# Kernel optimization log

Measured on AMD Instinct MI355X. Metric: run time of the kernel, lower is better.

Reference implementation:

```python
import jax, jax.numpy as jnp
import numpy as np

EXP_SCALE = 10.0   # self.exp_param_scale
BETA_UP = 5.0      # self.kernel_beta_upbound
N_HEAD = 12


def setup_inputs() -> dict:
    key = jax.random.key(0)
    ks = jax.random.split(key, 7)
    B, T, C, nh = 2, 2048, 768, N_HEAD
    s = 1.0 / np.sqrt(C)
    x = jax.random.normal(ks[0], (B, T, C), jnp.float32)
    W_la = jax.random.normal(ks[1], (C, C), jnp.float32) * s      # LeakyAverage linear
    la_coef = jax.random.uniform(ks[2], (nh,), jnp.float32)        # per-head leaky decay in (0,1)
    W_v = jax.random.normal(ks[3], (C, C), jnp.float32) * s        # v_featurizer linear
    v_coef = jax.random.uniform(ks[4], (nh,), jnp.float32)         # v_featurizer per-head coef
    kernel_beta = jnp.ones((nh,), jnp.float32) / EXP_SCALE
    value_beta = jnp.ones((nh,), jnp.float32) * (-0.5 / EXP_SCALE)
    W_proj = jax.random.normal(ks[5], (C, C), jnp.float32) * s     # c_proj
    return dict(x=x, W_la=W_la, la_coef=la_coef, W_v=W_v, v_coef=v_coef,
                kernel_beta=kernel_beta, value_beta=value_beta, W_proj=W_proj)


def _leaky_average(x, W_la, la_coef):
    # y_t = c * y_{t-1} + (1-c) * (x W^T)_t, per-head decay c. Returns (B, nh, T, hs).
    B, T, C = x.shape
    nh = la_coef.shape[0]
    hs = C // nh
    u = (x @ W_la.T).reshape(B, T, nh, hs)
    c = la_coef[None, :, None]  # (1, nh, 1) broadcast over (B, nh, hs)

    def step(carry, ut):
        y = c * carry + (1.0 - c) * ut
        return y, y

    _, ys = jax.lax.scan(step, jnp.zeros((B, nh, hs), x.dtype), jnp.swapaxes(u, 0, 1))
    return jnp.transpose(ys, (1, 2, 0, 3))  # (T,B,nh,hs) -> (B,nh,T,hs)


def reference(x, W_la, la_coef, W_v, v_coef, kernel_beta, value_beta, W_proj):
    B, T, C = x.shape
    nh = la_coef.shape[0]
    hs = C // nh
    v_shift = 1

    # K path: leaky-average features, L2-normalize, exp-kernel beta scale
    k0 = _leaky_average(x, W_la, la_coef)                               # (B,nh,T,hs)
    raw_k = k0 / (jnp.linalg.norm(k0, axis=-1, keepdims=True) + 1e-6)
    beta = jnp.exp(jnp.minimum(kernel_beta * EXP_SCALE, BETA_UP))
    k = raw_k * beta[None, :, None, None]

    # V path: lowrlinearconv featurizer (linear, shift-by-1 mix, normalize) + value scale
    xl = (x @ W_v.T).reshape(B, T, nh, hs).transpose(0, 2, 1, 3)        # (B,nh,T,hs)
    shifted = jnp.concatenate([xl[:, :, 1:], jnp.zeros_like(xl[:, :, :1])], axis=2)
    vc = v_coef[None, :, None, None]
    vf = shifted * (1.0 - vc) + xl * vc
    vf = vf / (jnp.linalg.norm(vf, axis=-1, keepdims=True) + 1e-6)
    vbeta = jnp.exp(jnp.minimum(value_beta * EXP_SCALE, BETA_UP))
    v = vf * vbeta[None, :, None, None]

    # shifted-causal attention: query at position t (t>=1) attends keys 0..t-1, scale=1.0
    q = k[:, :, v_shift:]                                               # (B,nh,T-1,hs)
    scores = jnp.einsum('bhqd,bhkd->bhqk', q, k)                        # (B,nh,T-1,T)
    mask = jnp.tril(jnp.ones((T - v_shift, T), bool))                   # j <= iq  <=>  key < query pos
    scores = jnp.where(mask, scores, -jnp.inf)
    attn = jax.nn.softmax(scores, axis=-1)
    o = jnp.einsum('bhqk,bhkd->bhqd', attn, v)
    y = jnp.concatenate([jnp.zeros((B, nh, v_shift, hs), x.dtype), o], axis=2)

    y = y.transpose(0, 2, 1, 3).reshape(B, T, C)
    return y @ W_proj.T  # c_proj (dropouts are identity in eval)
```

## Files before the change

kernel.cpp:

```cpp
#include <hip/hip_runtime.h>
#include <hip/hip_bf16.h>
#include <math.h>

#define B_   2
#define T_   2048
#define C_   768
#define NH   12
#define HS   64
#define NSEG 64
#define SEGLEN 32
#define CX   1536

typedef __attribute__((ext_vector_type(8))) short short8;
typedef __attribute__((ext_vector_type(4))) short short4v;
typedef __attribute__((ext_vector_type(4))) float f32x4;

static __device__ inline unsigned short f2b(float f) {
  __hip_bfloat16 h = __float2bfloat16(f);
  unsigned short u;
  __builtin_memcpy(&u, &h, 2);
  return u;
}

#define GLOAD_LDS16(gp, lp)                                                        \
  __builtin_amdgcn_global_load_lds((const __attribute__((address_space(1))) void*)(gp), \
                                   (__attribute__((address_space(3))) void*)(lp), 16, 0, 0)

__global__ __launch_bounds__(256) void cast_all(const float* __restrict__ x,
                                                const float* __restrict__ wla,
                                                const float* __restrict__ wv,
                                                const float* __restrict__ wp,
                                                __hip_bfloat16* __restrict__ xb,
                                                __hip_bfloat16* __restrict__ wcat,
                                                __hip_bfloat16* __restrict__ wpb) {
  const int NX4 = (B_ * T_ * C_) / 4;
  const int NW4 = (C_ * C_) / 4;
  const int TOT = NX4 + 3 * NW4;
  int i = blockIdx.x * 256 + threadIdx.x;
  int st = gridDim.x * 256;
  for (; i < TOT; i += st) {
    const float* s;
    unsigned short* d;
    if (i < NX4) { s = x + (size_t)i * 4; d = (unsigned short*)xb + (size_t)i * 4; }
    else if (i < NX4 + NW4) { int j = i - NX4; s = wla + (size_t)j * 4; d = (unsigned short*)wcat + (size_t)j * 4; }
    else if (i < NX4 + 2 * NW4) { int j = i - NX4 - NW4; s = wv + (size_t)j * 4; d = (unsigned short*)wcat + (size_t)(C_ * C_) + (size_t)j * 4; }
    else { int j = i - NX4 - 2 * NW4; s = wp + (size_t)j * 4; d = (unsigned short*)wpb + (size_t)j * 4; }
    float4 v = *(const float4*)s;
    short4v o;
    o.x = (short)f2b(v.x); o.y = (short)f2b(v.y); o.z = (short)f2b(v.z); o.w = (short)f2b(v.w);
    *(short4v*)d = o;
  }
}

template <int BM>
__global__ __launch_bounds__(256) void gemm_bf16(const __hip_bfloat16* __restrict__ A,
                                                 const __hip_bfloat16* __restrict__ Bw,
                                                 float* __restrict__ C,
                                                 int M, int N, int K) {
  __shared__ __hip_bfloat16 As[BM * 64];
  __shared__ __hip_bfloat16 Bs[128 * 64];
  const int tid = threadIdx.x;
  const int w = tid >> 6, lane = tid & 63;
  const int bm = blockIdx.x * BM, bn = blockIdx.y * 128;
  const int q16 = lane & 15, lg = lane >> 4;

  constexpr int NACC = (BM == 128) ? 4 : 2;
  f32x4 acc[4][NACC];
#pragma unroll
  for (int i = 0; i < 4; ++i)
#pragma unroll
    for (int j = 0; j < NACC; ++j) acc[i][j] = (f32x4){0.f, 0.f, 0.f, 0.f};

  const int srow = (lane >> 3);
  const int soff0 = (lane & 7) * 16;
  const int sw = (lane & 7) << 4;
  constexpr int ACH = BM / 8;
  constexpr int CPW = (ACH + 16) / 4;

  for (int k0 = 0; k0 < K; k0 += 64) {
    __syncthreads();
#pragma unroll
    for (int c = 0; c < CPW; ++c) {
      int gc = w * CPW + c;
      int isB = gc >= ACH;
      int ci = isB ? gc - ACH : gc;
      int row = ci * 8 + srow;
      int soff = soff0 ^ ((row & 7) << 4);
      const __hip_bfloat16* gp =
          (isB ? Bw + (size_t)(bn + row) * K : A + (size_t)(bm + row) * K) + k0 + (soff >> 1);
      __hip_bfloat16* lp = (isB ? Bs : As) + ci * 512;
      GLOAD_LDS16(gp, lp);
    }
    __syncthreads();
#pragma unroll
    for (int ks = 0; ks < 2; ++ks) {
      short8 af[4], bf[NACC];
      const int colb = ks * 64 + lg * 16;
#pragma unroll
      for (int i = 0; i < 4; ++i) {
        int ra = (BM == 128) ? ((w >> 1) * 64 + i * 16 + q16) : (i * 16 + q16);
        af[i] = *(const short8*)((const char*)As + ra * 128 + (colb ^ sw));
      }
#pragma unroll
      for (int j = 0; j < NACC; ++j) {
        int rb = (BM == 128) ? ((w & 1) * 64 + j * 16 + q16) : (w * 32 + j * 16 + q16);
        bf[j] = *(const short8*)((const char*)Bs + rb * 128 + (colb ^ sw));
      }
#pragma unroll
      for (int i = 0; i < 4; ++i)
#pragma unroll
        for (int j = 0; j < NACC; ++j)
          acc[i][j] = __builtin_amdgcn_mfma_f32_16x16x32_bf16(af[i], bf[j], acc[i][j], 0, 0, 0);
    }
  }
#pragma unroll
  for (int i = 0; i < 4; ++i) {
#pragma unroll
    for (int r = 0; r < 4; ++r) {
      int m = (BM == 128) ? (bm + (w >> 1) * 64 + i * 16 + lg * 4 + r)
                          : (bm + i * 16 + lg * 4 + r);
      int nb = (BM == 128) ? (bn + (w & 1) * 64 + q16) : (bn + w * 32 + q16);
      float* cp = C + (size_t)m * N + nb;
#pragma unroll
      for (int j = 0; j < NACC; ++j) cp[j * 16] = acc[i][j][r];
    }
  }
}

__global__ __launch_bounds__(256) void scan_seg(const float* __restrict__ uxv,
                                                const float* __restrict__ la_coef,
                                                float* __restrict__ segend) {
  int cid = blockIdx.x * 4 + (threadIdx.x >> 6);
  int d   = threadIdx.x & 63;
  int seg = cid & (NSEG - 1);
  int bh  = cid >> 6;
  int h   = bh % NH;
  int b   = bh / NH;
  float c  = la_coef[h];
  float oc = 1.f - c;
  int t0 = seg * SEGLEN;
  const float* up = uxv + ((size_t)b * T_ + t0) * CX + h * HS + d;
  float y = 0.f;
  for (int i = 0; i < SEGLEN; ++i)
    y = fmaf(c, y, oc * up[(size_t)i * CX]);
  segend[(size_t)cid * HS + d] = y;
}

__global__ __launch_bounds__(256) void scan_b(const float* __restrict__ la_coef,
                                              const float* __restrict__ segend,
                                              float* __restrict__ carryin) {
  int s = blockIdx.x * 256 + threadIdx.x;
  if (s >= B_ * NH * HS) return;
  int d  = s & 63;
  int bh = s >> 6;
  int h  = bh % NH;
  float c = la_coef[h];
  float cl = c;
#pragma unroll
  for (int i = 0; i < 5; ++i) cl *= cl;
  float h0 = 0.f;
  for (int seg = 0; seg < NSEG; ++seg) {
    int cid = bh * NSEG + seg;
    carryin[(size_t)cid * HS + d] = h0;
    h0 = fmaf(cl, h0, segend[(size_t)cid * HS + d]);
  }
}

__global__ __launch_bounds__(256) void scan_c_norm(const float* __restrict__ la_coef,
                                                   const float* __restrict__ kernel_beta,
                                                   const float* __restrict__ carryin,
                                                   const float* __restrict__ uxv,
                                                   __hip_bfloat16* __restrict__ kb16) {
  int cid = blockIdx.x * 4 + (threadIdx.x >> 6);
  int d   = threadIdx.x & 63;
  int seg = cid & (NSEG - 1);
  int bh  = cid >> 6;
  int h   = bh % NH;
  int b   = bh / NH;
  float c  = la_coef[h];
  float oc = 1.f - c;
  float bk = __expf(fminf(kernel_beta[h] * 10.f, 5.f));
  int t0 = seg * SEGLEN;
  const float* up = uxv + ((size_t)b * T_ + t0) * CX + h * HS + d;
  __hip_bfloat16* op = kb16 + ((size_t)bh * T_ + t0) * HS + d;
  float y = carryin[(size_t)cid * HS + d];
  for (int i = 0; i < SEGLEN; ++i) {
    y = fmaf(c, y, oc * up[(size_t)i * CX]);
    float ss = y * y;
#pragma unroll
    for (int off = 1; off < 64; off <<= 1) ss += __shfl_xor(ss, off, 64);
    float scale = bk / (sqrtf(ss) + 1e-6f);
    op[(size_t)i * HS] = __float2bfloat16(y * scale);
  }
}

__global__ __launch_bounds__(256) void vbuild_t(const float* __restrict__ uxv,
                                                const float* __restrict__ v_coef,
                                                const float* __restrict__ value_beta,
                                                __hip_bfloat16* __restrict__ vt) {
  __shared__ __hip_bfloat16 sm[64][73];
  int t0 = blockIdx.x * 64;
  int bh = blockIdx.y;
  int h = bh % NH, b = bh / NH;
  int w = threadIdx.x >> 6, lane = threadIdx.x & 63;
  float vc = v_coef[h];
  float vb = __expf(fminf(value_beta[h] * 10.f, 5.f));
  for (int i = 0; i < 16; ++i) {
    int tl = w * 16 + i;
    int t = t0 + tl;
    const float* xp = uxv + ((size_t)b * T_ + t) * CX + 768 + h * HS + lane;
    float x0 = *xp;
    float x1 = (t + 1 < T_) ? xp[CX] : 0.f;
    float vf = (1.f - vc) * x1 + vc * x0;
    float ss = vf * vf;
#pragma unroll
    for (int off = 1; off < 64; off <<= 1) ss += __shfl_xor(ss, off, 64);
    sm[tl][lane] = __float2bfloat16(vf * vb / (sqrtf(ss) + 1e-6f));
  }
  __syncthreads();
  int d = threadIdx.x >> 3;
  int c = threadIdx.x & 7;
  for (int i = 0; i < 2; ++i) {
    int dd = d + i * 32;
    short8 v;
#pragma unroll
    for (int k = 0; k < 8; ++k)
      v[k] = (short)((const unsigned short*)&sm[c * 8 + k][dd])[0];
    *(short8*)((unsigned short*)vt + ((size_t)bh * HS + dd) * T_ + t0 + c * 8) = v;
  }
}

__global__ __launch_bounds__(256, 4) void attn7(const __hip_bfloat16* __restrict__ Kg,
                                                const __hip_bfloat16* __restrict__ Vtg,
                                                const float* __restrict__ kernel_beta,
                                                __hip_bfloat16* __restrict__ Y) {
  __shared__ __hip_bfloat16 Kt[2][64 * 64];
  __shared__ __hip_bfloat16 Vt[3][64 * 64];
  __shared__ char Pl[4][2304];
  const int bh = blockIdx.x;
  const int b = bh / NH, h = bh % NH;
  const int w = threadIdx.x >> 6, lane = threadIdx.x & 63;
  const int q16 = lane & 15, lg = lane >> 4;
  const int it = 31 - blockIdx.y;
  const int qb0 = 1 + it * 64;
  float bk = __expf(fminf(kernel_beta[h] * 10.f, 5.f));
  float m0 = bk * bk;
  const unsigned short* Kh = (const unsigned short*)Kg + (size_t)bh * T_ * HS;
  const unsigned short* Vh = (const unsigned short*)Vtg + (size_t)bh * HS * T_;
  unsigned short* Yh = (unsigned short*)Y + (size_t)b * T_ * C_ + h * HS;

  if (it == 0 && w == 0) Yh[lane] = 0;

  const int tq = qb0 + w * 16 + q16;
  short8 qf[2];
  {
    int tqc = tq > T_ - 1 ? T_ - 1 : tq;
#pragma unroll
    for (int ks = 0; ks < 2; ++ks)
      qf[ks] = *(const short8*)(Kh + (size_t)tqc * HS + ks * 32 + lg * 8);
  }

  f32x4 zero = {0.f, 0.f, 0.f, 0.f};
  f32x4 accO[4];
#pragma unroll
  for (int mt = 0; mt < 4; ++mt) accO[mt] = zero;
  float lsum = 0.f;
  f32x4 sp[4];

  char* pb = &Pl[w][0] + q16 * 144;
  const int swr = (q16 & 7) << 4;

  const int srow = lane >> 3;
  const int soff = ((lane & 7) << 4) ^ (srow << 4);

  const int NT = (qb0 + 126) >> 6;

#define STAGE_KV(kbuf, vbuf, j0)                                                      \
  {                                                                                   \
    _Pragma("unroll")                                                                 \
    for (int n = 0; n < 2; ++n) {                                                     \
      int ch = w * 2 + n;                                                             \
      int row = ch * 8 + srow;                                                        \
      GLOAD_LDS16((const char*)(Kh + (size_t)((j0) + row) * HS) + soff,               \
                  &Kt[kbuf][ch * 512]);                                               \
      GLOAD_LDS16((const char*)(Vh + (size_t)row * T_ + (j0)) + soff,                 \
                  &Vt[vbuf][ch * 512]);                                               \
    }                                                                                 \
  }

#define SM_PV(tp)                                                                     \
  {                                                                                   \
    const int j0p = (tp)*64;                                                          \
    const char* Vb = (const char*)&Vt[(tp) % 3][0];                                   \
    _Pragma("unroll")                                                                 \
    for (int nt = 0; nt < 4; ++nt) {                                                  \
      float p[4];                                                                     \
      _Pragma("unroll")                                                               \
      for (int r = 0; r < 4; ++r) {                                                   \
        int j = j0p + nt * 16 + lg * 4 + r;                                           \
        p[r] = (j < tq) ? __expf(sp[nt][r] - m0) : 0.f;                               \
        lsum += p[r];                                                                 \
      }                                                                               \
      unsigned int w0, w1;                                                            \
      asm("v_cvt_pk_bf16_f32 %0, %1, %2" : "=v"(w0) : "v"(p[0]), "v"(p[1]));          \
      asm("v_cvt_pk_bf16_f32 %0, %1, %2" : "=v"(w1) : "v"(p[2]), "v"(p[3]));          \
      uint2 pk; pk.x = w0; pk.y = w1;                                                 \
      *(uint2*)(pb + nt * 32 + lg * 8) = pk;                                          \
    }                                                                                 \
    __builtin_amdgcn_s_setprio(1);                                                    \
    _Pragma("unroll")                                                                 \
    for (int ks = 0; ks < 2; ++ks) {                                                  \
      short8 pf = *(const short8*)(pb + ks * 64 + lg * 16);                           \
      _Pragma("unroll")                                                               \
      for (int mt = 0; mt < 4; ++mt) {                                                \
        short8 vf = *(const short8*)(Vb + (mt * 16 + q16) * 128 +                     \
                                     ((ks * 64 + lg * 16) ^ swr));                    \
        accO[mt] = __builtin_amdgcn_mfma_f32_16x16x32_bf16(vf, pf, accO[mt], 0, 0, 0);\
      }                                                                               \
    }                                                                                 \
    __builtin_amdgcn_s_setprio(0);                                                    \
  }

  STAGE_KV(0, 0, 0);

  for (int kt = 0; kt < NT; ++kt) {
    const int j0 = kt * 64;
    if (kt + 1 < NT) {
      STAGE_KV((kt + 1) & 1, (kt + 1) % 3, j0 + 64);
      asm volatile("s_waitcnt vmcnt(4)" ::: "memory");
    } else {
      asm volatile("s_waitcnt vmcnt(0)" ::: "memory");
    }
    __builtin_amdgcn_s_barrier();
    __builtin_amdgcn_sched_barrier(0);

    const char* Kb = (const char*)&Kt[kt & 1][0];
    short8 kf[4][2];
#pragma unroll
    for (int nt = 0; nt < 4; ++nt)
#pragma unroll
      for (int ks = 0; ks < 2; ++ks)
        kf[nt][ks] = *(const short8*)(Kb + (nt * 16 + q16) * 128 + ((ks * 64 + lg * 16) ^ swr));
    f32x4 sc[4];
    __builtin_amdgcn_s_setprio(1);
#pragma unroll
    for (int nt = 0; nt < 4; ++nt) {
      sc[nt] = __builtin_amdgcn_mfma_f32_16x16x32_bf16(kf[nt][0], qf[0], zero, 0, 0, 0);
      sc[nt] = __builtin_amdgcn_mfma_f32_16x16x32_bf16(kf[nt][1], qf[1], sc[nt], 0, 0, 0);
    }
    __builtin_amdgcn_s_setprio(0);

    if (kt > 0) SM_PV(kt - 1);

#pragma unroll
    for (int nt = 0; nt < 4; ++nt) sp[nt] = sc[nt];

    asm volatile("s_waitcnt lgkmcnt(0)" ::: "memory");
    __builtin_amdgcn_s_barrier();
  }
  SM_PV(NT - 1);

  {
    float v = lsum;
    v += __shfl_xor(v, 16, 64);
    v += __shfl_xor(v, 32, 64);
    float inv = 1.f / v;
    if (tq < T_) {
      unsigned short* yp = Yh + (size_t)tq * C_;
#pragma unroll
      for (int mt = 0; mt < 4; ++mt) {
        float o0 = accO[mt][0] * inv, o1 = accO[mt][1] * inv;
        float o2 = accO[mt][2] * inv, o3 = accO[mt][3] * inv;
        unsigned int u0, u1;
        asm("v_cvt_pk_bf16_f32 %0, %1, %2" : "=v"(u0) : "v"(o0), "v"(o1));
        asm("v_cvt_pk_bf16_f32 %0, %1, %2" : "=v"(u1) : "v"(o2), "v"(o3));
        uint2 pk; pk.x = u0; pk.y = u1;
        *(uint2*)(yp + mt * 16 + lg * 4) = pk;
      }
    }
  }
#undef STAGE_KV
#undef SM_PV
}

extern "C" void kernel_launch(void* const* d_in, const int* in_sizes, int n_in,
                              void* d_out, int out_size, void* d_ws, size_t ws_size,
                              hipStream_t stream) {
  const float* x          = (const float*)d_in[0];
  const float* W_la       = (const float*)d_in[1];
  const float* la_coef    = (const float*)d_in[2];
  const float* W_v        = (const float*)d_in[3];
  const float* v_coef     = (const float*)d_in[4];
  const float* kernel_bet = (const float*)d_in[5];
  const float* value_bet  = (const float*)d_in[6];
  const float* W_proj     = (const float*)d_in[7];
  float* out = (float*)d_out;

  float* ws = (float*)d_ws;
  const size_t NTOK = (size_t)B_ * T_ * C_;
  const size_t NSEGTOT = (size_t)B_ * NH * NSEG * HS;
  float* uxv     = ws;
  float* segend  = uxv + (size_t)B_ * T_ * CX;
  float* carryin = segend + NSEGTOT;
  __hip_bfloat16* kb16 = (__hip_bfloat16*)(carryin + NSEGTOT);
  __hip_bfloat16* vt16 = kb16 + NTOK;
  __hip_bfloat16* xb   = vt16 + NTOK;
  __hip_bfloat16* Wcat = xb + NTOK;
  __hip_bfloat16* Wpb  = Wcat + (size_t)CX * C_;
  __hip_bfloat16* yb   = xb;

  const int M = B_ * T_;

  cast_all<<<2048, 256, 0, stream>>>(x, W_la, W_v, W_proj, xb, Wcat, Wpb);

  gemm_bf16<64><<<dim3(M / 64, CX / 128), 256, 0, stream>>>(xb, Wcat, uxv, M, CX, C_);

  scan_seg<<<dim3(B_ * NH * NSEG / 4), 256, 0, stream>>>(uxv, la_coef, segend);
  scan_b<<<dim3((B_ * NH * HS + 255) / 256), 256, 0, stream>>>(la_coef, segend, carryin);
  scan_c_norm<<<dim3(B_ * NH * NSEG / 4), 256, 0, stream>>>(la_coef, kernel_bet, carryin, uxv, kb16);

  vbuild_t<<<dim3(T_ / 64, B_ * NH), 256, 0, stream>>>(uxv, v_coef, value_bet, vt16);

  attn7<<<dim3(B_ * NH, 32), 256, 0, stream>>>(kb16, vt16, kernel_bet, yb);

  gemm_bf16<64><<<dim3(M / 64, C_ / 128), 256, 0, stream>>>(yb, Wpb, out, M, C_, C_);
}
```

Measured before the change: 110.7 us.

## Store projection output as bf16, fuse scan and V-build kernels, use exp2

The first GEMM now writes its 4096x1536 projection as bf16 instead of fp32, which halves the intermediate traffic read by the scan and V-building kernels. The scan kernels preload a whole segment into registers so the loads can overlap. The final scan pass and the V builder are merged into one launch whose blocks branch on their index, removing a kernel launch and letting the two jobs share the device. The attention softmax switches to exp2 with a fused multiply-add. The cost is extra rounding of the leaky-average and V inputs to bf16 before the recurrence.

```diff
diff --git a/kernel.cpp b/kernel.cpp
--- a/kernel.cpp
+++ b/kernel.cpp
@@ -20,6 +20,12 @@
   unsigned short u;
   __builtin_memcpy(&u, &h, 2);
   return u;
+}
+static __device__ inline float b2f(unsigned short u) {
+  unsigned int x = ((unsigned int)u) << 16;
+  float f;
+  __builtin_memcpy(&f, &x, 4);
+  return f;
 }
 
 #define GLOAD_LDS16(gp, lp)                                                        \
@@ -52,10 +58,10 @@
   }
 }
 
-template <int BM>
+template <int BM, bool OB16>
 __global__ __launch_bounds__(256) void gemm_bf16(const __hip_bfloat16* __restrict__ A,
                                                  const __hip_bfloat16* __restrict__ Bw,
-                                                 float* __restrict__ C,
+                                                 void* __restrict__ Cv,
                                                  int M, int N, int K) {
   __shared__ __hip_bfloat16 As[BM * 64];
   __shared__ __hip_bfloat16 Bs[128 * 64];
@@ -120,14 +126,20 @@
       int m = (BM == 128) ? (bm + (w >> 1) * 64 + i * 16 + lg * 4 + r)
                           : (bm + i * 16 + lg * 4 + r);
       int nb = (BM == 128) ? (bn + (w & 1) * 64 + q16) : (bn + w * 32 + q16);
-      float* cp = C + (size_t)m * N + nb;
-#pragma unroll
-      for (int j = 0; j < NACC; ++j) cp[j * 16] = acc[i][j][r];
-    }
-  }
-}
-
-__global__ __launch_bounds__(256) void scan_seg(const float* __restrict__ uxv,
+      if (OB16) {
+        unsigned short* cp = (unsigned short*)Cv + (size_t)m * N + nb;
+#pragma unroll
+        for (int j = 0; j < NACC; ++j) cp[j * 16] = f2b(acc[i][j][r]);
+      } else {
+        float* cp = (float*)Cv + (size_t)m * N + nb;
+#pragma unroll
+        for (int j = 0; j < NACC; ++j) cp[j * 16] = acc[i][j][r];
+      }
+    }
+  }
+}
+
+__global__ __launch_bounds__(256) void scan_seg(const unsigned short* __restrict__ uxv,
                                                 const float* __restrict__ la_coef,
                                                 float* __restrict__ segend) {
   int cid = blockIdx.x * 4 + (threadIdx.x >> 6);
@@ -139,10 +151,13 @@
   float c  = la_coef[h];
   float oc = 1.f - c;
   int t0 = seg * SEGLEN;
-  const float* up = uxv + ((size_t)b * T_ + t0) * CX + h * HS + d;
+  const unsigned short* up = uxv + ((size_t)b * T_ + t0) * CX + h * HS + d;
+  float uv[SEGLEN];
+#pragma unroll
+  for (int i = 0; i < SEGLEN; ++i) uv[i] = b2f(up[(size_t)i * CX]);
   float y = 0.f;
-  for (int i = 0; i < SEGLEN; ++i)
-    y = fmaf(c, y, oc * up[(size_t)i * CX]);
+#pragma unroll
+  for (int i = 0; i < SEGLEN; ++i) y = fmaf(c, y, oc * uv[i]);
   segend[(size_t)cid * HS + d] = y;
 }
 
@@ -166,67 +181,72 @@
   }
 }
 
-__global__ __launch_bounds__(256) void scan_c_norm(const float* __restrict__ la_coef,
-                                                   const float* __restrict__ kernel_beta,
-                                                   const float* __restrict__ carryin,
-                                                   const float* __restrict__ uxv,
-                                                   __hip_bfloat16* __restrict__ kb16) {
-  int cid = blockIdx.x * 4 + (threadIdx.x >> 6);
-  int d   = threadIdx.x & 63;
-  int seg = cid & (NSEG - 1);
-  int bh  = cid >> 6;
-  int h   = bh % NH;
-  int b   = bh / NH;
-  float c  = la_coef[h];
-  float oc = 1.f - c;
-  float bk = __expf(fminf(kernel_beta[h] * 10.f, 5.f));
-  int t0 = seg * SEGLEN;
-  const float* up = uxv + ((size_t)b * T_ + t0) * CX + h * HS + d;
-  __hip_bfloat16* op = kb16 + ((size_t)bh * T_ + t0) * HS + d;
-  float y = carryin[(size_t)cid * HS + d];
-  for (int i = 0; i < SEGLEN; ++i) {
-    y = fmaf(c, y, oc * up[(size_t)i * CX]);
-    float ss = y * y;
-#pragma unroll
-    for (int off = 1; off < 64; off <<= 1) ss += __shfl_xor(ss, off, 64);
-    float scale = bk / (sqrtf(ss) + 1e-6f);
-    op[(size_t)i * HS] = __float2bfloat16(y * scale);
-  }
-}
-
-__global__ __launch_bounds__(256) void vbuild_t(const float* __restrict__ uxv,
-                                                const float* __restrict__ v_coef,
-                                                const float* __restrict__ value_beta,
-                                                __hip_bfloat16* __restrict__ vt) {
+__global__ __launch_bounds__(256) void scanc_vbuild(const float* __restrict__ la_coef,
+                                                    const float* __restrict__ kernel_beta,
+                                                    const float* __restrict__ carryin,
+                                                    const unsigned short* __restrict__ uxv,
+                                                    const float* __restrict__ v_coef,
+                                                    const float* __restrict__ value_beta,
+                                                    __hip_bfloat16* __restrict__ kb16,
+                                                    __hip_bfloat16* __restrict__ vt) {
   __shared__ __hip_bfloat16 sm[64][73];
-  int t0 = blockIdx.x * 64;
-  int bh = blockIdx.y;
-  int h = bh % NH, b = bh / NH;
-  int w = threadIdx.x >> 6, lane = threadIdx.x & 63;
-  float vc = v_coef[h];
-  float vb = __expf(fminf(value_beta[h] * 10.f, 5.f));
-  for (int i = 0; i < 16; ++i) {
-    int tl = w * 16 + i;
-    int t = t0 + tl;
-    const float* xp = uxv + ((size_t)b * T_ + t) * CX + 768 + h * HS + lane;
-    float x0 = *xp;
-    float x1 = (t + 1 < T_) ? xp[CX] : 0.f;
-    float vf = (1.f - vc) * x1 + vc * x0;
-    float ss = vf * vf;
-#pragma unroll
-    for (int off = 1; off < 64; off <<= 1) ss += __shfl_xor(ss, off, 64);
-    sm[tl][lane] = __float2bfloat16(vf * vb / (sqrtf(ss) + 1e-6f));
-  }
-  __syncthreads();
-  int d = threadIdx.x >> 3;
-  int c = threadIdx.x & 7;
-  for (int i = 0; i < 2; ++i) {
-    int dd = d + i * 32;
-    short8 v;
-#pragma unroll
-    for (int k = 0; k < 8; ++k)
-      v[k] = (short)((const unsigned short*)&sm[c * 8 + k][dd])[0];
-    *(short8*)((unsigned short*)vt + ((size_t)bh * HS + dd) * T_ + t0 + c * 8) = v;
+  const int NBC = B_ * NH * NSEG / 4;
+  if ((int)blockIdx.x < NBC) {
+    int cid = blockIdx.x * 4 + (threadIdx.x >> 6);
+    int d   = threadIdx.x & 63;
+    int seg = cid & (NSEG - 1);
+    int bh  = cid >> 6;
+    int h   = bh % NH;
+    int b   = bh / NH;
+    float c  = la_coef[h];
+    float oc = 1.f - c;
+    float bk = __expf(fminf(kernel_beta[h] * 10.f, 5.f));
+    int t0 = seg * SEGLEN;
+    const unsigned short* up = uxv + ((size_t)b * T_ + t0) * CX + h * HS + d;
+    __hip_bfloat16* op = kb16 + ((size_t)bh * T_ + t0) * HS + d;
+    float uv[SEGLEN];
+#pragma unroll
+    for (int i = 0; i < SEGLEN; ++i) uv[i] = b2f(up[(size_t)i * CX]);
+    float y = carryin[(size_t)cid * HS + d];
+    for (int i = 0; i < SEGLEN; ++i) {
+      y = fmaf(c, y, oc * uv[i]);
+      float ss = y * y;
+#pragma unroll
+      for (int off = 1; off < 64; off <<= 1) ss += __shfl_xor(ss, off, 64);
+      float scale = bk / (sqrtf(ss) + 1e-6f);
+      op[(size_t)i * HS] = __float2bfloat16(y * scale);
+    }
+  } else {
+    int idx = blockIdx.x - NBC;
+    int t0 = (idx & 31) * 64;
+    int bh = idx >> 5;
+    int h = bh % NH, b = bh / NH;
+    int w = threadIdx.x >> 6, lane = threadIdx.x & 63;
+    float vc = v_coef[h];
+    float vb = __expf(fminf(value_beta[h] * 10.f, 5.f));
+    for (int i = 0; i < 16; ++i) {
+      int tl = w * 16 + i;
+      int t = t0 + tl;
+      const unsigned short* xp = uxv + ((size_t)b * T_ + t) * CX + 768 + h * HS + lane;
+      float x0 = b2f(*xp);
+      float x1 = (t + 1 < T_) ? b2f(xp[CX]) : 0.f;
+      float vf = (1.f - vc) * x1 + vc * x0;
+      float ss = vf * vf;
+#pragma unroll
+      for (int off = 1; off < 64; off <<= 1) ss += __shfl_xor(ss, off, 64);
+      sm[tl][lane] = __float2bfloat16(vf * vb / (sqrtf(ss) + 1e-6f));
+    }
+    __syncthreads();
+    int d = threadIdx.x >> 3;
+    int c = threadIdx.x & 7;
+    for (int i = 0; i < 2; ++i) {
+      int dd = d + i * 32;
+      short8 v;
+#pragma unroll
+      for (int k = 0; k < 8; ++k)
+        v[k] = (short)((const unsigned short*)&sm[c * 8 + k][dd])[0];
+      *(short8*)((unsigned short*)vt + ((size_t)bh * HS + dd) * T_ + t0 + c * 8) = v;
+    }
   }
 }
 
@@ -244,7 +264,8 @@
   const int it = 31 - blockIdx.y;
   const int qb0 = 1 + it * 64;
   float bk = __expf(fminf(kernel_beta[h] * 10.f, 5.f));
-  float m0 = bk * bk;
+  const float L2E = 1.4426950408889634f;
+  float m0l = bk * bk * L2E;
   const unsigned short* Kh = (const unsigned short*)Kg + (size_t)bh * T_ * HS;
   const unsigned short* Vh = (const unsigned short*)Vtg + (size_t)bh * HS * T_;
   unsigned short* Yh = (unsigned short*)Y + (size_t)b * T_ * C_ + h * HS;
@@ -298,7 +319,7 @@
       _Pragma("unroll")                                                               \
       for (int r = 0; r < 4; ++r) {                                                   \
         int j = j0p + nt * 16 + lg * 4 + r;                                           \
-        p[r] = (j < tq) ? __expf(sp[nt][r] - m0) : 0.f;                               \
+        p[r] = (j < tq) ? exp2f(fmaf(sp[nt][r], L2E, -m0l)) : 0.f;                    \
         lsum += p[r];                                                                 \
       }                                                                               \
       unsigned int w0, w1;                                                            \
@@ -396,11 +417,11 @@
   const float* W_proj     = (const float*)d_in[7];
   float* out = (float*)d_out;
 
-  float* ws = (float*)d_ws;
+  char* ws = (char*)d_ws;
   const size_t NTOK = (size_t)B_ * T_ * C_;
   const size_t NSEGTOT = (size_t)B_ * NH * NSEG * HS;
-  float* uxv     = ws;
-  float* segend  = uxv + (size_t)B_ * T_ * CX;
+  unsigned short* uxv = (unsigned short*)ws;
+  float* segend  = (float*)(ws + (size_t)B_ * T_ * CX * 2);
   float* carryin = segend + NSEGTOT;
   __hip_bfloat16* kb16 = (__hip_bfloat16*)(carryin + NSEGTOT);
   __hip_bfloat16* vt16 = kb16 + NTOK;
@@ -413,15 +434,14 @@
 
   cast_all<<<2048, 256, 0, stream>>>(x, W_la, W_v, W_proj, xb, Wcat, Wpb);
 
-  gemm_bf16<64><<<dim3(M / 64, CX / 128), 256, 0, stream>>>(xb, Wcat, uxv, M, CX, C_);
+  gemm_bf16<64, true><<<dim3(M / 64, CX / 128), 256, 0, stream>>>(xb, Wcat, uxv, M, CX, C_);
 
   scan_seg<<<dim3(B_ * NH * NSEG / 4), 256, 0, stream>>>(uxv, la_coef, segend);
   scan_b<<<dim3((B_ * NH * HS + 255) / 256), 256, 0, stream>>>(la_coef, segend, carryin);
-  scan_c_norm<<<dim3(B_ * NH * NSEG / 4), 256, 0, stream>>>(la_coef, kernel_bet, carryin, uxv, kb16);
-
-  vbuild_t<<<dim3(T_ / 64, B_ * NH), 256, 0, stream>>>(uxv, v_coef, value_bet, vt16);
+  scanc_vbuild<<<dim3(B_ * NH * NSEG / 4 + 32 * B_ * NH), 256, 0, stream>>>(
+      la_coef, kernel_bet, carryin, uxv, v_coef, value_bet, kb16, vt16);
 
   attn7<<<dim3(B_ * NH, 32), 256, 0, stream>>>(kb16, vt16, kernel_bet, yb);
 
-  gemm_bf16<64><<<dim3(M / 64, C_ / 128), 256, 0, stream>>>(yb, Wpb, out, M, C_, C_);
-}
+  gemm_bf16<64, false><<<dim3(M / 64, C_ / 128), 256, 0, stream>>>(yb, Wpb, out, M, C_, C_);
+}
```

Result: faster. 104.4 us (-5.7%).
